# Kernel optimization log

Hardware: AMD Instinct MI355X
Metric: run time of the kernel (lower is better)

The kernel has to match this reference:

```python
import jax, jax.numpy as jnp
import numpy as np

D = 512

def _layernorm(x, g, b, eps=1e-5):
    m = jnp.mean(x, axis=-1, keepdims=True)
    v = jnp.mean((x - m) ** 2, axis=-1, keepdims=True)
    return (x - m) / jnp.sqrt(v + eps) * g + b

def _bn_eval(x, g, b, eps=1e-5):
    # BatchNorm1d in eval mode with fresh buffers: running_mean=0, running_var=1
    return x / jnp.sqrt(1.0 + eps) * g + b

def setup_inputs() -> dict:
    key = jax.random.key(0)
    ks = jax.random.split(key, 8)
    B, V = 4096, 20
    s = 0.02
    return {
        "x":   jax.random.normal(ks[0], (B * V, D), jnp.float32),
        "We":  jax.random.normal(ks[1], (D, D), jnp.float32) * s,
        "be":  jnp.zeros((D,), jnp.float32),
        "W1":  jax.random.normal(ks[2], (D, D), jnp.float32) * s,
        "b1":  jnp.zeros((D,), jnp.float32),
        "Wa":  jax.random.normal(ks[3], (D, 1), jnp.float32) * s,
        "ba":  jnp.zeros((1,), jnp.float32),
        "W2":  jax.random.normal(ks[4], (D, D), jnp.float32) * s,
        "b2":  jnp.zeros((D,), jnp.float32),
        "ln_g": jnp.ones((D,), jnp.float32),
        "ln_b": jnp.zeros((D,), jnp.float32),
        "h1W": jax.random.normal(ks[5], (D, D), jnp.float32) * s,
        "h1b": jnp.zeros((D,), jnp.float32),
        "bn1_g": jnp.ones((D,), jnp.float32),
        "bn1_b": jnp.zeros((D,), jnp.float32),
        "h2W": jax.random.normal(ks[6], (D, 256), jnp.float32) * s,
        "h2b": jnp.zeros((256,), jnp.float32),
        "bn2_g": jnp.ones((256,), jnp.float32),
        "bn2_b": jnp.zeros((256,), jnp.float32),
        "h3W": jax.random.normal(ks[7], (256, 40), jnp.float32) * s,
        "h3b": jnp.zeros((40,), jnp.float32),
        "num_views": 20,
        "group_num": 8,
    }

def reference(x, We, be, W1, b1, Wa, ba, W2, b2, ln_g, ln_b,
              h1W, h1b, bn1_g, bn1_b, h2W, h2b, bn2_g, bn2_b, h3W, h3b,
              num_views, group_num):
    V = num_views
    f_cnn = x @ We + be                                  # [B*V, 512] stand-in encoder
    B = f_cnn.shape[0] // V
    xv = f_cnn.reshape(B, V, D)
    x1 = xv @ W1 + b1                                    # mlp1, [B, V, 512]
    f_vit1 = _layernorm(x1, ln_g, ln_b)
    att = jax.nn.sigmoid(f_vit1 @ Wa + ba)               # [B, V, 1], scores in (0,1)
    # group_pooling: bucket views by floor(score*group_num), max-pool per bucket,
    # then the forward takes max over the (non-empty) bucket maxes -- which is
    # exactly the max over all views of x1 (every view lands in one bucket).
    # bucket = clip(floor(att*group_num), 0, group_num-1)  # target for fused kernel
    f_vit2 = jnp.max(x1, axis=1)                         # [B, 512]
    f_vit2 = _layernorm(f_vit2 @ W2 + b2, ln_g, ln_b)    # mlp2 + shared norm
    h = _bn_eval(f_vit2 @ h1W + h1b, bn1_g, bn1_b)       # cls_head_finetune[:2]
    f_global = h
    h = jax.nn.relu(h)                                   # dropout = identity (eval)
    h = jax.nn.relu(_bn_eval(h @ h2W + h2b, bn2_g, bn2_b))
    pred = h @ h3W + h3b                                 # [B, 40]
    return (f_cnn.reshape(-1, D), f_vit1.reshape(-1, D), att.reshape(-1, V),
            f_vit2, f_global, pred)
```

## Files before the change

### kernel.cpp

```cpp
#include <hip/hip_runtime.h>
#include <cstdint>

typedef unsigned short u16;
typedef __bf16 bf16x8 __attribute__((ext_vector_type(8)));
typedef float f32x4 __attribute__((ext_vector_type(4)));

#define GLOBAL_AS __attribute__((address_space(1)))
#define LDS_AS __attribute__((address_space(3)))

__device__ __forceinline__ u16 f2bf(float f) {
  unsigned u = __builtin_bit_cast(unsigned, f);
  u += 0x7FFFu + ((u >> 16) & 1u);
  return (u16)(u >> 16);
}
__device__ __forceinline__ float bf2f(u16 h) {
  unsigned u = ((unsigned)h) << 16;
  return __builtin_bit_cast(float, u);
}
__device__ __forceinline__ void unpack2(unsigned u, float& a, float& b) {
  a = __builtin_bit_cast(float, u << 16);
  b = __builtin_bit_cast(float, u & 0xFFFF0000u);
}
__device__ __forceinline__ unsigned pk2(float a, float b) {
  return (unsigned)f2bf(a) | ((unsigned)f2bf(b) << 16);
}
__device__ __forceinline__ void gl_lds16(const void* g, void* l) {
  __builtin_amdgcn_global_load_lds((const GLOBAL_AS void*)g, (LDS_AS void*)l, 16, 0, 0);
}

__global__ __launch_bounds__(256) void transpose_w(const float* __restrict__ W,
                                                   u16* __restrict__ Wt, int K, int N) {
  __shared__ float tile[32][33];
  const int n0 = blockIdx.x * 32, k0 = blockIdx.y * 32;
  const int tx = threadIdx.x & 31, ty = threadIdx.x >> 5;
#pragma unroll
  for (int i = 0; i < 32; i += 8)
    tile[ty + i][tx] = W[(size_t)(k0 + ty + i) * N + n0 + tx];
  __syncthreads();
#pragma unroll
  for (int i = 0; i < 32; i += 8)
    Wt[(size_t)(n0 + ty + i) * K + k0 + tx] = f2bf(tile[tx][ty + i]);
}

__global__ __launch_bounds__(128) void bias_c(const float* __restrict__ be,
                                              const float* __restrict__ W1,
                                              const float* __restrict__ b1,
                                              float* __restrict__ bc) {
  const int n = blockIdx.x * 128 + threadIdx.x;
  float s = b1[n];
  for (int k = 0; k < 512; ++k) s += be[k] * W1[(size_t)k * 512 + n];
  bc[n] = s;
}

template <int MODE, int FM, int FN, bool AF32>
__global__ __launch_bounds__(256) void gemm_k2(
    const float* __restrict__ Af, const u16* __restrict__ Ab,
    const u16* __restrict__ Bt, const float* __restrict__ bias,
    float* __restrict__ outF, u16* __restrict__ outB,
    const float* __restrict__ bng, const float* __restrict__ bnb, int N) {
  constexpr int TM = 32 * FM, TN = 32 * FN;
  __shared__ __align__(16) u16 As[2][TM * 32];
  __shared__ __align__(16) u16 Bs[2][TN * 32];
  const int t = threadIdx.x;
  const int tn0 = blockIdx.x * TN, tm0 = blockIdx.y * TM;
  const int w = t >> 6, lane = t & 63;
  const int wm = w >> 1, wn = w & 1, lr = lane & 15, quad = lane >> 4;

  f32x4 acc[FM][FN];
#pragma unroll
  for (int i = 0; i < FM; ++i)
#pragma unroll
    for (int j = 0; j < FN; ++j) {
      acc[i][j][0] = 0.f; acc[i][j][1] = 0.f; acc[i][j][2] = 0.f; acc[i][j][3] = 0.f;
    }

  float4 aq[4];
  auto stage = [&](int buf, int kb) {
#pragma unroll
    for (int i = 0; i < TN / 64; ++i) {
      const int c = t + 256 * i;
      gl_lds16(Bt + (size_t)(tn0 + (c >> 2)) * 512 + kb + (c & 3) * 8, &Bs[buf][c * 8]);
    }
    if constexpr (!AF32) {
#pragma unroll
      for (int i = 0; i < TM / 64; ++i) {
        const int c = t + 256 * i;
        gl_lds16(Ab + (size_t)(tm0 + (c >> 2)) * 512 + kb + (c & 3) * 8, &As[buf][c * 8]);
      }
    }
  };
  auto loadA = [&](int kb) {
    const int row = t >> 1, half = t & 1;
    const float* g = Af + (size_t)(tm0 + row) * 512 + kb + half * 16;
    aq[0] = ((const float4*)g)[0]; aq[1] = ((const float4*)g)[1];
    aq[2] = ((const float4*)g)[2]; aq[3] = ((const float4*)g)[3];
  };
  auto writeA = [&](int buf) {
    const int row = t >> 1, half = t & 1;
    int4 s0 = make_int4(pk2(aq[0].x, aq[0].y), pk2(aq[0].z, aq[0].w),
                        pk2(aq[1].x, aq[1].y), pk2(aq[1].z, aq[1].w));
    int4 s1 = make_int4(pk2(aq[2].x, aq[2].y), pk2(aq[2].z, aq[2].w),
                        pk2(aq[3].x, aq[3].y), pk2(aq[3].z, aq[3].w));
    const int m = (row & 7) << 3;
    *(int4*)&As[buf][(row * 32 + half * 16) ^ m] = s0;
    *(int4*)&As[buf][(row * 32 + half * 16 + 8) ^ m] = s1;
  };

  if constexpr (AF32) { loadA(0); writeA(0); }
  stage(0, 0);
  __syncthreads();

  for (int kc = 0; kc < 16; ++kc) {
    const int cur = kc & 1;
    if (kc < 15) {
      if constexpr (AF32) loadA(kc * 32 + 32);
      stage(cur ^ 1, kc * 32 + 32);
    }
    bf16x8 af[FM], bfr[FN];
#pragma unroll
    for (int mt = 0; mt < FM; ++mt) {
      const int ar = wm * (TM / 2) + mt * 16 + lr;
      const int idx = AF32 ? ((ar * 32 + quad * 8) ^ ((ar & 7) << 3)) : (ar * 32 + quad * 8);
      af[mt] = *(const bf16x8*)&As[cur][idx];
    }
#pragma unroll
    for (int nt = 0; nt < FN; ++nt)
      bfr[nt] = *(const bf16x8*)&Bs[cur][(wn * (TN / 2) + nt * 16 + lr) * 32 + quad * 8];
#pragma unroll
    for (int mt = 0; mt < FM; ++mt)
#pragma unroll
      for (int nt = 0; nt < FN; ++nt)
        acc[mt][nt] = __builtin_amdgcn_mfma_f32_16x16x32_bf16(af[mt], bfr[nt], acc[mt][nt], 0, 0, 0);
    if (kc < 15) {
      if constexpr (AF32) writeA(cur ^ 1);
    }
    __syncthreads();
  }

  const float BNS = 0.9999950000374998f;
#pragma unroll
  for (int nt = 0; nt < FN; ++nt) {
    const int col = tn0 + wn * (TN / 2) + nt * 16 + lr;
    float bs = 0.f, g_ = 0.f, b_ = 0.f;
    if constexpr (MODE != 7) bs = bias[col];
    if constexpr (MODE == 2 || MODE == 3) { g_ = bng[col] * BNS; b_ = bnb[col]; }
#pragma unroll
    for (int mt = 0; mt < FM; ++mt) {
      const int row0 = tm0 + wm * (TM / 2) + mt * 16 + quad * 4;
#pragma unroll
      for (int r = 0; r < 4; ++r) {
        const float v = acc[mt][nt][r] + bs;
        if constexpr (MODE == 1) {
          outF[(size_t)(row0 + r) * N + col] = v;
        } else if constexpr (MODE == 2) {
          const float y = v * g_ + b_;
          const size_t idx = (size_t)(row0 + r) * N + col;
          outF[idx] = y;
          outB[idx] = f2bf(fmaxf(y, 0.f));
        } else if constexpr (MODE == 3) {
          const float y = v * g_ + b_;
          outB[(size_t)(row0 + r) * N + col] = f2bf(fmaxf(y, 0.f));
        } else {
          outB[(size_t)col * N + (row0 + r)] = f2bf(v);
        }
      }
    }
  }
}

__global__ __launch_bounds__(256) void gemm_x2(
    const float* __restrict__ x, const u16* __restrict__ B1t, const u16* __restrict__ B2t,
    const float* __restrict__ b1v, const float* __restrict__ b2v,
    float* __restrict__ outF, u16* __restrict__ outB) {
  __shared__ __align__(16) u16 As[2][128 * 32];
  __shared__ __align__(16) u16 B1s[2][128 * 32];
  __shared__ __align__(16) u16 B2s[2][128 * 32];
  const int t = threadIdx.x;
  int bid = blockIdx.y * 4 + blockIdx.x;
  bid = (bid & 7) * 320 + (bid >> 3);
  const int tn0 = (bid & 3) * 128, tm0 = (bid >> 2) * 128;
  const int w = t >> 6, lane = t & 63;
  const int wm = w >> 1, wn = w & 1, lr = lane & 15, quad = lane >> 4;

  f32x4 acc0[4][4], acc1[4][4];
#pragma unroll
  for (int i = 0; i < 4; ++i)
#pragma unroll
    for (int j = 0; j < 4; ++j) {
      acc0[i][j][0] = 0.f; acc0[i][j][1] = 0.f; acc0[i][j][2] = 0.f; acc0[i][j][3] = 0.f;
      acc1[i][j][0] = 0.f; acc1[i][j][1] = 0.f; acc1[i][j][2] = 0.f; acc1[i][j][3] = 0.f;
    }

  float4 aq[4];
  auto stageB = [&](int buf, int kb) {
#pragma unroll
    for (int i = 0; i < 2; ++i) {
      const int c = t + 256 * i;
      const size_t go = (size_t)(tn0 + (c >> 2)) * 512 + kb + (c & 3) * 8;
      gl_lds16(B1t + go, &B1s[buf][c * 8]);
      gl_lds16(B2t + go, &B2s[buf][c * 8]);
    }
  };
  auto loadA = [&](int kb) {
    const int row = t >> 1, half = t & 1;
    const float* g = x + (size_t)(tm0 + row) * 512 + kb + half * 16;
    aq[0] = ((const float4*)g)[0]; aq[1] = ((const float4*)g)[1];
    aq[2] = ((const float4*)g)[2]; aq[3] = ((const float4*)g)[3];
  };
  auto writeA = [&](int buf) {
    const int row = t >> 1, half = t & 1;
    int4 s0 = make_int4(pk2(aq[0].x, aq[0].y), pk2(aq[0].z, aq[0].w),
                        pk2(aq[1].x, aq[1].y), pk2(aq[1].z, aq[1].w));
    int4 s1 = make_int4(pk2(aq[2].x, aq[2].y), pk2(aq[2].z, aq[2].w),
                        pk2(aq[3].x, aq[3].y), pk2(aq[3].z, aq[3].w));
    const int m = (row & 7) << 3;
    *(int4*)&As[buf][(row * 32 + half * 16) ^ m] = s0;
    *(int4*)&As[buf][(row * 32 + half * 16 + 8) ^ m] = s1;
  };

  loadA(0); writeA(0); stageB(0, 0);
  __syncthreads();

  for (int kc = 0; kc < 16; ++kc) {
    const int cur = kc & 1;
    if (kc < 15) {
      loadA(kc * 32 + 32);
      stageB(cur ^ 1, kc * 32 + 32);
    }
    bf16x8 af[4];
#pragma unroll
    for (int mt = 0; mt < 4; ++mt) {
      const int ar = wm * 64 + mt * 16 + lr;
      af[mt] = *(const bf16x8*)&As[cur][(ar * 32 + quad * 8) ^ ((ar & 7) << 3)];
    }
#pragma unroll
    for (int nt = 0; nt < 4; ++nt) {
      const int bi = (wn * 64 + nt * 16 + lr) * 32 + quad * 8;
      bf16x8 b1 = *(const bf16x8*)&B1s[cur][bi];
#pragma unroll
      for (int mt = 0; mt < 4; ++mt)
        acc0[mt][nt] = __builtin_amdgcn_mfma_f32_16x16x32_bf16(af[mt], b1, acc0[mt][nt], 0, 0, 0);
      bf16x8 b2 = *(const bf16x8*)&B2s[cur][bi];
#pragma unroll
      for (int mt = 0; mt < 4; ++mt)
        acc1[mt][nt] = __builtin_amdgcn_mfma_f32_16x16x32_bf16(af[mt], b2, acc1[mt][nt], 0, 0, 0);
    }
    if (kc < 15) writeA(cur ^ 1);
    __syncthreads();
  }

#pragma unroll
  for (int nt = 0; nt < 4; ++nt) {
    const int col = tn0 + wn * 64 + nt * 16 + lr;
    const float bsE = b1v[col], bsC = b2v[col];
#pragma unroll
    for (int mt = 0; mt < 4; ++mt) {
      const int row0 = tm0 + wm * 64 + mt * 16 + quad * 4;
#pragma unroll
      for (int r = 0; r < 4; ++r) {
        const size_t idx = (size_t)(row0 + r) * 512 + col;
        outF[idx] = acc0[mt][nt][r] + bsE;
        outB[idx] = f2bf(acc1[mt][nt][r] + bsC);
      }
    }
  }
}

__global__ __launch_bounds__(256) void fuse_ln_att_max(
    const u16* __restrict__ x1, const float* __restrict__ g, const float* __restrict__ bb,
    const float* __restrict__ Wa, const float* __restrict__ ba,
    float* __restrict__ fv1, float* __restrict__ att, u16* __restrict__ fv2raw) {
  __shared__ __align__(16) u16 xs[20 * 512];
  const int b = blockIdx.x, t = threadIdx.x;
  const int4* src = (const int4*)(x1 + (size_t)b * 10240);
  int4* dst = (int4*)xs;
#pragma unroll
  for (int i = 0; i < 5; ++i) dst[t + 256 * i] = src[t + 256 * i];
  __syncthreads();
  const int w = t >> 6, lane = t & 63;
  const float inv512 = 1.0f / 512.0f;
  const float ba0 = ba[0];
  float gv[8], bv[8], wv[8];
#pragma unroll
  for (int e = 0; e < 8; ++e) {
    gv[e] = g[lane * 8 + e];
    bv[e] = bb[lane * 8 + e];
    wv[e] = Wa[lane * 8 + e];
  }
#pragma unroll
  for (int j = 0; j < 5; ++j) {
    const int v = w * 5 + j;
    int4 q = *(const int4*)&xs[v * 512 + lane * 8];
    float f[8];
    unpack2((unsigned)q.x, f[0], f[1]);
    unpack2((unsigned)q.y, f[2], f[3]);
    unpack2((unsigned)q.z, f[4], f[5]);
    unpack2((unsigned)q.w, f[6], f[7]);
    float s = 0.f, ss = 0.f;
#pragma unroll
    for (int e = 0; e < 8; ++e) { s += f[e]; ss += f[e] * f[e]; }
#pragma unroll
    for (int o = 32; o; o >>= 1) { s += __shfl_xor(s, o); ss += __shfl_xor(ss, o); }
    const float m = s * inv512;
    const float var = ss * inv512 - m * m;
    const float rs = rsqrtf(var + 1e-5f);
    float y[8], z = 0.f;
#pragma unroll
    for (int e = 0; e < 8; ++e) {
      y[e] = (f[e] - m) * rs * gv[e] + bv[e];
      z += y[e] * wv[e];
    }
    float* op = fv1 + ((size_t)b * 20 + v) * 512 + lane * 8;
    *(float4*)op = make_float4(y[0], y[1], y[2], y[3]);
    *(float4*)(op + 4) = make_float4(y[4], y[5], y[6], y[7]);
#pragma unroll
    for (int o = 32; o; o >>= 1) z += __shfl_xor(z, o);
    if (lane == 0) att[(size_t)b * 20 + v] = 1.f / (1.f + __expf(-(z + ba0)));
  }
  for (int d = t; d < 512; d += 256) {
    float mx = -3.4e38f;
#pragma unroll
    for (int v = 0; v < 20; ++v) mx = fmaxf(mx, bf2f(xs[v * 512 + d]));
    fv2raw[(size_t)b * 512 + d] = f2bf(mx);
  }
}

__global__ __launch_bounds__(256) void ln_rows(const float* __restrict__ in,
                                               const float* __restrict__ g,
                                               const float* __restrict__ bb,
                                               float* __restrict__ outF, u16* __restrict__ outB) {
  const int row = blockIdx.x * 4 + (threadIdx.x >> 6);
  const int lane = threadIdx.x & 63;
  const float* p = in + (size_t)row * 512 + lane * 8;
  float4 a = *(const float4*)p, c = *(const float4*)(p + 4);
  float f[8] = {a.x, a.y, a.z, a.w, c.x, c.y, c.z, c.w};
  float s = 0.f, ss = 0.f;
#pragma unroll
  for (int e = 0; e < 8; ++e) { s += f[e]; ss += f[e] * f[e]; }
#pragma unroll
  for (int o = 32; o; o >>= 1) { s += __shfl_xor(s, o); ss += __shfl_xor(ss, o); }
  const float m = s * (1.0f / 512.0f);
  const float rs = rsqrtf(ss * (1.0f / 512.0f) - m * m + 1e-5f);
  float y[8];
#pragma unroll
  for (int e = 0; e < 8; ++e) y[e] = (f[e] - m) * rs * g[lane * 8 + e] + bb[lane * 8 + e];
  float* op = outF + (size_t)row * 512 + lane * 8;
  *(float4*)op = make_float4(y[0], y[1], y[2], y[3]);
  *(float4*)(op + 4) = make_float4(y[4], y[5], y[6], y[7]);
  int4 ob = make_int4(pk2(y[0], y[1]), pk2(y[2], y[3]), pk2(y[4], y[5]), pk2(y[6], y[7]));
  *(int4*)(outB + (size_t)row * 512 + lane * 8) = ob;
}

__global__ __launch_bounds__(320) void pred_k(const u16* __restrict__ h2a,
                                              const float* __restrict__ W,
                                              const float* __restrict__ bias,
                                              float* __restrict__ out) {
  const int t = threadIdx.x;
  const int r = t / 40, n = t - r * 40;
  const size_t b = (size_t)blockIdx.x * 8 + r;
  const u16* hp = h2a + b * 256;
  float s = 0.f;
#pragma unroll 4
  for (int k0 = 0; k0 < 256; k0 += 8) {
    int4 q = *(const int4*)(hp + k0);
    float f0, f1, f2, f3, f4, f5, f6, f7;
    unpack2((unsigned)q.x, f0, f1);
    unpack2((unsigned)q.y, f2, f3);
    unpack2((unsigned)q.z, f4, f5);
    unpack2((unsigned)q.w, f6, f7);
    const float* wp = W + (size_t)k0 * 40 + n;
    s += f0 * wp[0] + f1 * wp[40] + f2 * wp[80] + f3 * wp[120] +
         f4 * wp[160] + f5 * wp[200] + f6 * wp[240] + f7 * wp[280];
  }
  out[b * 40 + n] = s + bias[n];
}

extern "C" void kernel_launch(void* const* d_in, const int* in_sizes, int n_in,
                              void* d_out, int out_size, void* d_ws, size_t ws_size,
                              hipStream_t stream) {
  (void)in_sizes; (void)n_in; (void)out_size; (void)ws_size;
  const float* x    = (const float*)d_in[0];
  const float* We   = (const float*)d_in[1];
  const float* be   = (const float*)d_in[2];
  const float* W1   = (const float*)d_in[3];
  const float* b1   = (const float*)d_in[4];
  const float* Wa   = (const float*)d_in[5];
  const float* ba   = (const float*)d_in[6];
  const float* W2   = (const float*)d_in[7];
  const float* b2   = (const float*)d_in[8];
  const float* ln_g = (const float*)d_in[9];
  const float* ln_b = (const float*)d_in[10];
  const float* h1W  = (const float*)d_in[11];
  const float* h1b  = (const float*)d_in[12];
  const float* bn1g = (const float*)d_in[13];
  const float* bn1b = (const float*)d_in[14];
  const float* h2W  = (const float*)d_in[15];
  const float* h2b  = (const float*)d_in[16];
  const float* bn2g = (const float*)d_in[17];
  const float* bn2b = (const float*)d_in[18];
  const float* h3W  = (const float*)d_in[19];
  const float* h3b  = (const float*)d_in[20];

  float* out = (float*)d_out;
  float* o_fcnn  = out;
  float* o_fvit1 = o_fcnn + 41943040;
  float* o_att   = o_fvit1 + 41943040;
  float* o_fvit2 = o_att + 81920;
  float* o_fglob = o_fvit2 + 2097152;
  float* o_pred  = o_fglob + 2097152;

  u16* ws = (u16*)d_ws;
  u16* Wet   = ws;
  u16* W1t   = Wet + 262144;
  u16* W2t   = W1t + 262144;
  u16* h1Wt  = W2t + 262144;
  u16* h2Wt  = h1Wt + 262144;
  u16* Wct   = h2Wt + 131072;
  u16* x1B   = Wct + 262144;
  u16* fv2rB = x1B + 41943040;
  u16* fv2B  = fv2rB + 2097152;
  u16* hrelB = fv2B + 2097152;
  u16* h2aB  = hrelB + 2097152;
  float* bc    = (float*)(h2aB + 1048576);
  float* t3raw = bc + 512;

  const dim3 blk(256);
  transpose_w<<<dim3(16, 16), blk, 0, stream>>>(We, Wet, 512, 512);
  transpose_w<<<dim3(16, 16), blk, 0, stream>>>(W1, W1t, 512, 512);
  transpose_w<<<dim3(16, 16), blk, 0, stream>>>(W2, W2t, 512, 512);
  transpose_w<<<dim3(16, 16), blk, 0, stream>>>(h1W, h1Wt, 512, 512);
  transpose_w<<<dim3(8, 16), blk, 0, stream>>>(h2W, h2Wt, 512, 256);

  gemm_k2<7, 4, 4, true><<<dim3(4, 4), blk, 0, stream>>>(
      We, nullptr, W1t, nullptr, nullptr, Wct, nullptr, nullptr, 512);
  bias_c<<<dim3(4), dim3(128), 0, stream>>>(be, W1, b1, bc);

  gemm_x2<<<dim3(4, 640), blk, 0, stream>>>(x, Wet, Wct, be, bc, o_fcnn, x1B);

  fuse_ln_att_max<<<dim3(4096), blk, 0, stream>>>(x1B, ln_g, ln_b, Wa, ba, o_fvit1, o_att, fv2rB);

  gemm_k2<1, 2, 2, false><<<dim3(8, 64), blk, 0, stream>>>(
      nullptr, fv2rB, W2t, b2, t3raw, nullptr, nullptr, nullptr, 512);
  ln_rows<<<dim3(1024), blk, 0, stream>>>(t3raw, ln_g, ln_b, o_fvit2, fv2B);
  gemm_k2<2, 2, 2, false><<<dim3(8, 64), blk, 0, stream>>>(
      nullptr, fv2B, h1Wt, h1b, o_fglob, hrelB, bn1g, bn1b, 512);
  gemm_k2<3, 2, 2, false><<<dim3(4, 64), blk, 0, stream>>>(
      nullptr, hrelB, h2Wt, h2b, nullptr, h2aB, bn2g, bn2b, 256);
  pred_k<<<dim3(512), dim3(320), 0, stream>>>(h2aB, h3W, h3b, o_pred);
}
```

Before: 764.5 us.

## Pre-convert x to bf16 and split dual-output GEMM into N-concatenated tiles

Result: no change. 779.8 us (+2.0%).

```diff
diff --git a/kernel.cpp b/kernel.cpp
--- a/kernel.cpp
+++ b/kernel.cpp
@@ -26,6 +26,17 @@
 }
 __device__ __forceinline__ void gl_lds16(const void* g, void* l) {
   __builtin_amdgcn_global_load_lds((const GLOBAL_AS void*)g, (LDS_AS void*)l, 16, 0, 0);
+}
+
+__global__ __launch_bounds__(256) void xcvt(const float* __restrict__ x,
+                                            u16* __restrict__ xB, int n8) {
+  const int stride = gridDim.x * 256;
+  for (int i = blockIdx.x * 256 + threadIdx.x; i < n8; i += stride) {
+    const float4 a = ((const float4*)x)[(size_t)i * 2];
+    const float4 b = ((const float4*)x)[(size_t)i * 2 + 1];
+    int4 o = make_int4(pk2(a.x, a.y), pk2(a.z, a.w), pk2(b.x, b.y), pk2(b.z, b.w));
+    ((int4*)xB)[i] = o;
+  }
 }
 
 __global__ __launch_bounds__(256) void transpose_w(const float* __restrict__ W,
@@ -168,99 +179,68 @@
   }
 }
 
-__global__ __launch_bounds__(256) void gemm_x2(
-    const float* __restrict__ x, const u16* __restrict__ B1t, const u16* __restrict__ B2t,
-    const float* __restrict__ b1v, const float* __restrict__ b2v,
+__global__ __launch_bounds__(256) void gemm_xc(
+    const u16* __restrict__ xB, const u16* __restrict__ Wet, const u16* __restrict__ Wct,
+    const float* __restrict__ be, const float* __restrict__ bc,
     float* __restrict__ outF, u16* __restrict__ outB) {
-  __shared__ __align__(16) u16 As[2][128 * 32];
-  __shared__ __align__(16) u16 B1s[2][128 * 32];
-  __shared__ __align__(16) u16 B2s[2][128 * 32];
+  __shared__ __align__(16) u16 As[128 * 32];
+  __shared__ __align__(16) u16 Bs[128 * 32];
   const int t = threadIdx.x;
-  int bid = blockIdx.y * 4 + blockIdx.x;
-  bid = (bid & 7) * 320 + (bid >> 3);
-  const int tn0 = (bid & 3) * 128, tm0 = (bid >> 2) * 128;
+  const int lin = blockIdx.y * 8 + blockIdx.x;
+  const int swz = (lin & 7) * 640 + (lin >> 3);
+  const int tn0 = (swz & 7) * 128;
+  const int tm0 = (swz >> 3) * 128;
+  const bool isF = (tn0 < 512);
+  const u16* Bt = isF ? (Wet + (size_t)tn0 * 512) : (Wct + (size_t)(tn0 - 512) * 512);
+  const float* bias = isF ? (be + tn0) : (bc + (tn0 - 512));
   const int w = t >> 6, lane = t & 63;
   const int wm = w >> 1, wn = w & 1, lr = lane & 15, quad = lane >> 4;
 
-  f32x4 acc0[4][4], acc1[4][4];
+  f32x4 acc[4][4];
 #pragma unroll
   for (int i = 0; i < 4; ++i)
 #pragma unroll
     for (int j = 0; j < 4; ++j) {
-      acc0[i][j][0] = 0.f; acc0[i][j][1] = 0.f; acc0[i][j][2] = 0.f; acc0[i][j][3] = 0.f;
-      acc1[i][j][0] = 0.f; acc1[i][j][1] = 0.f; acc1[i][j][2] = 0.f; acc1[i][j][3] = 0.f;
-    }
-
-  float4 aq[4];
-  auto stageB = [&](int buf, int kb) {
-#pragma unroll
-    for (int i = 0; i < 2; ++i) {
-      const int c = t + 256 * i;
-      const size_t go = (size_t)(tn0 + (c >> 2)) * 512 + kb + (c & 3) * 8;
-      gl_lds16(B1t + go, &B1s[buf][c * 8]);
-      gl_lds16(B2t + go, &B2s[buf][c * 8]);
-    }
-  };
-  auto loadA = [&](int kb) {
-    const int row = t >> 1, half = t & 1;
-    const float* g = x + (size_t)(tm0 + row) * 512 + kb + half * 16;
-    aq[0] = ((const float4*)g)[0]; aq[1] = ((const float4*)g)[1];
-    aq[2] = ((const float4*)g)[2]; aq[3] = ((const float4*)g)[3];
-  };
-  auto writeA = [&](int buf) {
-    const int row = t >> 1, half = t & 1;
-    int4 s0 = make_int4(pk2(aq[0].x, aq[0].y), pk2(aq[0].z, aq[0].w),
-                        pk2(aq[1].x, aq[1].y), pk2(aq[1].z, aq[1].w));
-    int4 s1 = make_int4(pk2(aq[2].x, aq[2].y), pk2(aq[2].z, aq[2].w),
-                        pk2(aq[3].x, aq[3].y), pk2(aq[3].z, aq[3].w));
-    const int m = (row & 7) << 3;
-    *(int4*)&As[buf][(row * 32 + half * 16) ^ m] = s0;
-    *(int4*)&As[buf][(row * 32 + half * 16 + 8) ^ m] = s1;
-  };
-
-  loadA(0); writeA(0); stageB(0, 0);
-  __syncthreads();
-
+      acc[i][j][0] = 0.f; acc[i][j][1] = 0.f; acc[i][j][2] = 0.f; acc[i][j][3] = 0.f;
+    }
+
+  const int c0 = t, c1 = t + 256;
   for (int kc = 0; kc < 16; ++kc) {
-    const int cur = kc & 1;
-    if (kc < 15) {
-      loadA(kc * 32 + 32);
-      stageB(cur ^ 1, kc * 32 + 32);
-    }
-    bf16x8 af[4];
-#pragma unroll
-    for (int mt = 0; mt < 4; ++mt) {
-      const int ar = wm * 64 + mt * 16 + lr;
-      af[mt] = *(const bf16x8*)&As[cur][(ar * 32 + quad * 8) ^ ((ar & 7) << 3)];
-    }
-#pragma unroll
-    for (int nt = 0; nt < 4; ++nt) {
-      const int bi = (wn * 64 + nt * 16 + lr) * 32 + quad * 8;
-      bf16x8 b1 = *(const bf16x8*)&B1s[cur][bi];
-#pragma unroll
-      for (int mt = 0; mt < 4; ++mt)
-        acc0[mt][nt] = __builtin_amdgcn_mfma_f32_16x16x32_bf16(af[mt], b1, acc0[mt][nt], 0, 0, 0);
-      bf16x8 b2 = *(const bf16x8*)&B2s[cur][bi];
-#pragma unroll
-      for (int mt = 0; mt < 4; ++mt)
-        acc1[mt][nt] = __builtin_amdgcn_mfma_f32_16x16x32_bf16(af[mt], b2, acc1[mt][nt], 0, 0, 0);
-    }
-    if (kc < 15) writeA(cur ^ 1);
+    const int kb = kc * 32;
+    gl_lds16(Bt + (size_t)(c0 >> 2) * 512 + kb + (c0 & 3) * 8, Bs + c0 * 8);
+    gl_lds16(Bt + (size_t)(c1 >> 2) * 512 + kb + (c1 & 3) * 8, Bs + c1 * 8);
+    gl_lds16(xB + (size_t)(tm0 + (c0 >> 2)) * 512 + kb + (c0 & 3) * 8, As + c0 * 8);
+    gl_lds16(xB + (size_t)(tm0 + (c1 >> 2)) * 512 + kb + (c1 & 3) * 8, As + c1 * 8);
     __syncthreads();
+    bf16x8 af[4], bfr[4];
+#pragma unroll
+    for (int mt = 0; mt < 4; ++mt)
+      af[mt] = *(const bf16x8*)&As[(wm * 64 + mt * 16 + lr) * 32 + quad * 8];
+#pragma unroll
+    for (int nt = 0; nt < 4; ++nt)
+      bfr[nt] = *(const bf16x8*)&Bs[(wn * 64 + nt * 16 + lr) * 32 + quad * 8];
+#pragma unroll
+    for (int mt = 0; mt < 4; ++mt)
+#pragma unroll
+      for (int nt = 0; nt < 4; ++nt)
+        acc[mt][nt] = __builtin_amdgcn_mfma_f32_16x16x32_bf16(af[mt], bfr[nt], acc[mt][nt], 0, 0, 0);
+    __syncthreads();
   }
 
 #pragma unroll
   for (int nt = 0; nt < 4; ++nt) {
-    const int col = tn0 + wn * 64 + nt * 16 + lr;
-    const float bsE = b1v[col], bsC = b2v[col];
+    const int cl = wn * 64 + nt * 16 + lr;
+    const float bs = bias[cl];
+    const int colF = tn0 + cl;
+    const int colB = tn0 - 512 + cl;
 #pragma unroll
     for (int mt = 0; mt < 4; ++mt) {
       const int row0 = tm0 + wm * 64 + mt * 16 + quad * 4;
 #pragma unroll
       for (int r = 0; r < 4; ++r) {
-        const size_t idx = (size_t)(row0 + r) * 512 + col;
-        outF[idx] = acc0[mt][nt][r] + bsE;
-        outB[idx] = f2bf(acc1[mt][nt][r] + bsC);
+        const float v = acc[mt][nt][r] + bs;
+        if (isF) outF[(size_t)(row0 + r) * 512 + colF] = v;
+        else     outB[(size_t)(row0 + r) * 512 + colB] = f2bf(v);
       }
     }
   }
@@ -416,7 +396,8 @@
   u16* h1Wt  = W2t + 262144;
   u16* h2Wt  = h1Wt + 262144;
   u16* Wct   = h2Wt + 131072;
-  u16* x1B   = Wct + 262144;
+  u16* xBv   = Wct + 262144;
+  u16* x1B   = xBv + 41943040;
   u16* fv2rB = x1B + 41943040;
   u16* fv2B  = fv2rB + 2097152;
   u16* hrelB = fv2B + 2097152;
@@ -425,6 +406,8 @@
   float* t3raw = bc + 512;
 
   const dim3 blk(256);
+  xcvt<<<dim3(2048), blk, 0, stream>>>(x, xBv, 5242880);
+
   transpose_w<<<dim3(16, 16), blk, 0, stream>>>(We, Wet, 512, 512);
   transpose_w<<<dim3(16, 16), blk, 0, stream>>>(W1, W1t, 512, 512);
   transpose_w<<<dim3(16, 16), blk, 0, stream>>>(W2, W2t, 512, 512);
@@ -435,7 +418,7 @@
       We, nullptr, W1t, nullptr, nullptr, Wct, nullptr, nullptr, 512);
   bias_c<<<dim3(4), dim3(128), 0, stream>>>(be, W1, b1, bc);
 
-  gemm_x2<<<dim3(4, 640), blk, 0, stream>>>(x, Wet, Wct, be, bc, o_fcnn, x1B);
+  gemm_xc<<<dim3(8, 640), blk, 0, stream>>>(xBv, Wet, Wct, be, bc, o_fcnn, x1B);
 
   fuse_ln_att_max<<<dim3(4096), blk, 0, stream>>>(x1B, ln_g, ln_b, Wa, ba, o_fvit1, o_att, fv2rB);
 
```
